# Optimization experiments

Hardware: AMD Instinct MI355X
Metric: run time of the kernel (lower is better)

The kernel has to match this reference:

```python
import jax, jax.numpy as jnp
import numpy as np

BATCH, SEQ, DIM, NH = 2, 4096, 1024, 16
HD = DIM // NH
BLOCK = 64


def setup_inputs() -> dict:
    key = jax.random.key(0)
    ks = jax.random.split(key, 8)
    x = jax.random.normal(ks[0], (BATCH, SEQ, DIM), dtype=jnp.float32)
    # standard RoPE tables: (seq, head_dim)
    inv_freq = 1.0 / (10000.0 ** (jnp.arange(0, HD, 2, dtype=jnp.float32) / HD))
    t = jnp.arange(SEQ, dtype=jnp.float32)
    freqs = jnp.outer(t, inv_freq)                      # (SEQ, HD//2)
    emb = jnp.concatenate([freqs, freqs], axis=-1)      # (SEQ, HD)
    cos, sin = jnp.cos(emb), jnp.sin(emb)
    s = 0.02
    wq = jax.random.normal(ks[1], (DIM, DIM), jnp.float32) * s
    wk = jax.random.normal(ks[2], (DIM, DIM), jnp.float32) * s
    wv = jax.random.normal(ks[3], (DIM, DIM), jnp.float32) * s
    wo = jax.random.normal(ks[4], (DIM, DIM), jnp.float32) * s
    A_log = jax.random.normal(ks[5], (NH,), jnp.float32) * 0.1
    w_dt_w = jax.random.normal(ks[6], (DIM, NH), jnp.float32) * s
    w_dt_b = jnp.zeros((NH,), jnp.float32)
    return {"x": x, "cos": cos, "sin": sin, "wq": wq, "wk": wk, "wv": wv,
            "wo": wo, "A_log": A_log, "w_dt_w": w_dt_w, "w_dt_b": w_dt_b}


def segsum(a):
    """a: (..., T) -> (..., T, T) lower-triangular segment sums, -inf above diag."""
    T = a.shape[-1]
    cs = jnp.cumsum(a, axis=-1)
    seg = cs[..., :, None] - cs[..., None, :]
    mask = jnp.tril(jnp.ones((T, T), dtype=bool))
    return jnp.where(mask, seg, -jnp.inf)


def rotate_half(t):
    t1, t2 = jnp.split(t, 2, axis=-1)
    return jnp.concatenate([-t2, t1], axis=-1)


def ssd(X, A, B, C, block_len):
    """Mamba-2 SSD chunked scan.
    X: (b,l,h,p)  A: (b,l,h)  B,C: (b,l,h,n)
    """
    b, l, h, p = X.shape
    c = l // block_len
    Xc = X.reshape(b, c, block_len, h, p)
    Bc = B.reshape(b, c, block_len, h, -1)
    Cc = C.reshape(b, c, block_len, h, -1)
    Ac = jnp.transpose(A.reshape(b, c, block_len, h), (0, 3, 1, 2))  # (b,h,c,l)
    A_cumsum = jnp.cumsum(Ac, axis=-1)
    # intra-chunk (diagonal block) output
    L = jnp.exp(segsum(Ac))                                          # (b,h,c,l,l)
    Y_diag = jnp.einsum('bclhn,bcshn,bhcls,bcshp->bclhp', Cc, Bc, L, Xc)
    # per-chunk states
    decay_states = jnp.exp(A_cumsum[:, :, :, -1:] - A_cumsum)        # (b,h,c,l)
    states = jnp.einsum('bclhn,bhcl,bclhp->bchpn', Bc, decay_states, Xc)
    init = jnp.zeros_like(states[:, :1])
    states = jnp.concatenate([init, states], axis=1)                 # (b,c+1,h,p,n)
    # inter-chunk recurrence (done as a 1-SS matmul over chunk axis)
    A_last = jnp.pad(A_cumsum[:, :, :, -1], ((0, 0), (0, 0), (1, 0)))
    decay_chunk = jnp.exp(segsum(A_last))                            # (b,h,c+1,c+1)
    new_states = jnp.einsum('bhzc,bchpn->bzhpn', decay_chunk, states)
    states, final_state = new_states[:, :-1], new_states[:, -1]
    # state -> output contribution
    state_decay_out = jnp.exp(A_cumsum)
    Y_off = jnp.einsum('bclhn,bchpn,bhcl->bclhp', Cc, states, state_decay_out)
    Y = (Y_diag + Y_off).reshape(b, l, h, p)
    return Y, final_state


def reference(x, cos, sin, wq, wk, wv, wo, A_log, w_dt_w, w_dt_b):
    b, l, dim = x.shape
    h = A_log.shape[0]
    d = dim // h
    xq = (x @ wq).reshape(b, l, h, d)
    xk = (x @ wk).reshape(b, l, h, d)
    xv = (x @ wv).reshape(b, l, h, d)
    cb = cos[None, :, None, :]
    sb = sin[None, :, None, :]
    xq = xq * cb + rotate_half(xq) * sb
    xk = xk * cb + rotate_half(xk) * sb
    dt = jax.nn.softplus(x @ w_dt_w + w_dt_b)           # (b,l,h)
    A = -jnp.exp(A_log)[None, None, :] * dt             # (b,l,h)
    X = xv * dt[..., None]                              # (b,l,h,d)
    Y, state = ssd(X, A, xk, xq, BLOCK)
    # replicate torch's transpose(1,2).view(b, l, -1) exactly:
    y = jnp.transpose(Y, (0, 2, 1, 3)).reshape(b, l, h * d)
    return y @ wo, state
```

## Files before the change

### kernel.cpp

```cpp
#include <hip/hip_runtime.h>


typedef __bf16 bf16x8 __attribute__((ext_vector_type(8)));
typedef float f32x4 __attribute__((ext_vector_type(4)));
typedef unsigned int u32x4 __attribute__((ext_vector_type(4)));
typedef unsigned short u16x8 __attribute__((ext_vector_type(8)));
typedef unsigned short u16x4 __attribute__((ext_vector_type(4)));

__device__ __forceinline__ unsigned short f2bf(float f) {
  unsigned int u = __builtin_bit_cast(unsigned int, f);
  u += 0x7fffu + ((u >> 16) & 1u);
  return (unsigned short)(u >> 16);
}
__device__ __forceinline__ float bf2f(unsigned short s) {
  unsigned int u = ((unsigned int)s) << 16;
  return __builtin_bit_cast(float, u);
}

#define GLOAD16(gp, lp)                                                \
  __builtin_amdgcn_global_load_lds(                                    \
      (const __attribute__((address_space(1))) void*)(gp),             \
      (__attribute__((address_space(3))) void*)(lp), 16, 0, 0)

__global__ __launch_bounds__(256) void prep_kernel(
    const float* __restrict__ x, unsigned short* __restrict__ x_bf,
    const float* __restrict__ wdt, unsigned short* __restrict__ wdt_bf,
    const float* __restrict__ w0, const float* __restrict__ w1,
    const float* __restrict__ w2, const float* __restrict__ w3,
    unsigned short* __restrict__ wt) {
  const int bx = blockIdx.x;
  const int tid = threadIdx.x;
  if (bx < 8192) {
    const int g = bx * 256 + tid;
    f32x4 v = *reinterpret_cast<const f32x4*>(x + (size_t)g * 4);
    u16x4 o;
    o.x = f2bf(v.x); o.y = f2bf(v.y); o.z = f2bf(v.z); o.w = f2bf(v.w);
    *reinterpret_cast<u16x4*>(x_bf + (size_t)g * 4) = o;
  } else if (bx < 8256) {
    const int g = (bx - 8192) * 256 + tid;
    const int n = g >> 10, k = g & 1023;
    wdt_bf[g] = f2bf(wdt[k * 16 + n]);
  } else {
    __shared__ float tile[32][33];
    const int t = bx - 8256;
    const int z = t >> 10, by = (t >> 5) & 31, bxx = t & 31;
    const float* w = (z == 0) ? w0 : (z == 1) ? w1 : (z == 2) ? w2 : w3;
    unsigned short* o = wt + (size_t)z * 1024 * 1024;
    const int tx = tid & 31, ty = tid >> 5;
#pragma unroll
    for (int i = 0; i < 4; ++i)
      tile[ty + i * 8][tx] = w[(size_t)(by * 32 + ty + i * 8) * 1024 + bxx * 32 + tx];
    __syncthreads();
#pragma unroll
    for (int i = 0; i < 4; ++i)
      o[(size_t)(bxx * 32 + ty + i * 8) * 1024 + by * 32 + tx] =
          f2bf(tile[tx][ty + i * 8]);
  }
}

__global__ __launch_bounds__(128) void dt_gemm_kernel(
    const unsigned short* __restrict__ A,
    const unsigned short* __restrict__ Bt,
    const float* __restrict__ bdt, float* __restrict__ dt) {
  __shared__ unsigned short As[2 * 1024];
  const int tid = threadIdx.x, lane = tid & 63, w = tid >> 6;
  const int m0 = blockIdx.x * 32;
  const unsigned short* ga =
      A + (size_t)(m0 + w * 16 + (lane >> 2)) * 1024 + (lane & 3) * 8;
  unsigned short* la = As + w * 1024;
  const int lr = lane & 15, lk = (lane >> 4) * 8;
  const unsigned short* gb = Bt + (size_t)lr * 1024 + lk;
  f32x4 acc = {};
  for (int kt = 0; kt < 1024; kt += 64) {
    GLOAD16(ga + kt, la);
    GLOAD16(ga + kt + 32, la + 512);
    bf16x8 bF0 = *reinterpret_cast<const bf16x8*>(gb + kt);
    bf16x8 bF1 = *reinterpret_cast<const bf16x8*>(gb + kt + 32);
    __syncthreads();
    bf16x8 aF0 = *reinterpret_cast<const bf16x8*>(&la[lr * 32 + lk]);
    bf16x8 aF1 = *reinterpret_cast<const bf16x8*>(&la[512 + lr * 32 + lk]);
    acc = __builtin_amdgcn_mfma_f32_16x16x32_bf16(aF0, bF0, acc, 0, 0, 0);
    acc = __builtin_amdgcn_mfma_f32_16x16x32_bf16(aF1, bF1, acc, 0, 0, 0);
    __syncthreads();
  }
  const int h = lr;
  const float bv = bdt[h];
#pragma unroll
  for (int r = 0; r < 4; ++r) {
    const int row = m0 + w * 16 + (lane >> 4) * 4 + r;
    const float a = acc[r] + bv;
    const float sp = (a > 0.f) ? (a + log1pf(expf(-a))) : log1pf(expf(a));
    dt[(size_t)row * 16 + h] = sp;
  }
}

template <int EPI>
__global__ __launch_bounds__(256) void gemm128_kernel(
    const unsigned short* __restrict__ A, const unsigned short* __restrict__ Bt,
    void* __restrict__ out0, unsigned short* __restrict__ out1,
    unsigned short* __restrict__ out2, const float* __restrict__ cosb,
    const float* __restrict__ sinb, const float* __restrict__ dtb) {
  __shared__ unsigned short As[128 * 64];
  __shared__ unsigned short Bs[128 * 64];
  const int tid = threadIdx.x, lane = tid & 63, w = tid >> 6;
  const int id = blockIdx.x + gridDim.x * blockIdx.y;
  const int cpx = (gridDim.x * gridDim.y) >> 3;
  const int swz = (id & 7) * cpx + (id >> 3);
  const int m0 = (swz / gridDim.x) * 128, n0 = (swz % gridDim.x) * 128;
  const int rw = lane >> 3;
  const int cu = ((lane & 7) ^ rw) * 8;
  const unsigned short* ga = A + (size_t)(m0 + w * 8 + rw) * 1024 + cu;
  const unsigned short* gb = Bt + (size_t)(n0 + w * 8 + rw) * 1024 + cu;
  unsigned short* la = As + (w * 8) * 64;
  unsigned short* lb = Bs + (w * 8) * 64;
  const int lr = lane & 15, lku = lane >> 4;
  const int wr = w >> 1, wc = w & 1;
  const int xr = lr & 7;
  f32x4 acc[4][4] = {};
  for (int kt = 0; kt < 1024; kt += 64) {
#pragma unroll
    for (int g = 0; g < 4; ++g) {
      GLOAD16(ga + kt + (size_t)(g * 32) * 1024, la + g * 32 * 64);
      GLOAD16(gb + kt + (size_t)(g * 32) * 1024, lb + g * 32 * 64);
    }
    __syncthreads();
#pragma unroll
    for (int kk = 0; kk < 2; ++kk) {
      const int un = (((kk * 4 + lku) ^ xr) * 8);
      bf16x8 aF[4], bF[4];
#pragma unroll
      for (int i = 0; i < 4; ++i) {
        aF[i] = *reinterpret_cast<const bf16x8*>(&As[(wr * 64 + i * 16 + lr) * 64 + un]);
        bF[i] = *reinterpret_cast<const bf16x8*>(&Bs[(wc * 64 + i * 16 + lr) * 64 + un]);
      }
#pragma unroll
      for (int i = 0; i < 4; ++i)
#pragma unroll
        for (int j = 0; j < 4; ++j)
          acc[i][j] = __builtin_amdgcn_mfma_f32_16x16x32_bf16(aF[i], bF[j], acc[i][j], 0, 0, 0);
    }
    __syncthreads();
  }
  const int r0 = m0 + wr * 64 + ((lane >> 4) << 2);
  if constexpr (EPI == 0) {
    float* O = (float*)out0;
    const int c0 = n0 + wc * 64 + lr;
#pragma unroll
    for (int i = 0; i < 4; ++i)
#pragma unroll
      for (int j = 0; j < 4; ++j)
#pragma unroll
        for (int r = 0; r < 4; ++r)
          O[(size_t)(r0 + i * 16 + r) * 1024 + c0 + j * 16] = acc[i][j][r];
  } else {
    const int col = n0 + wc * 64;
    if (col < 2048) {
      unsigned short* O = (col < 1024) ? (unsigned short*)out0 : out1;
      const int cbase = col & 1023;
#pragma unroll
      for (int i = 0; i < 4; ++i)
#pragma unroll
        for (int jj = 0; jj < 2; ++jj) {
          const int d1 = jj * 16 + lr;
#pragma unroll
          for (int r = 0; r < 4; ++r) {
            const int row = r0 + i * 16 + r;
            const int l = row & 4095;
            const float cv = cosb[(size_t)l * 64 + d1];
            const float sv = sinb[(size_t)l * 64 + d1];
            const float v1 = acc[i][jj][r], v2 = acc[i][jj + 2][r];
            O[(size_t)row * 1024 + cbase + jj * 16 + lr] = f2bf(v1 * cv - v2 * sv);
            O[(size_t)row * 1024 + cbase + jj * 16 + lr + 32] = f2bf(v2 * cv + v1 * sv);
          }
        }
    } else {
      unsigned short* O = out2;
      const int cbase = col - 2048;
      const int h = cbase >> 6;
#pragma unroll
      for (int i = 0; i < 4; ++i)
#pragma unroll
        for (int r = 0; r < 4; ++r) {
          const int row = r0 + i * 16 + r;
          const float dtv = dtb[(size_t)row * 16 + h];
#pragma unroll
          for (int j = 0; j < 4; ++j)
            O[(size_t)row * 1024 + cbase + j * 16 + lr] = f2bf(acc[i][j][r] * dtv);
        }
    }
  }
}

__global__ __launch_bounds__(256) void ssd_states_kernel(
    const unsigned short* __restrict__ Kb, const unsigned short* __restrict__ Xb,
    const float* __restrict__ dtb, const float* __restrict__ A_log,
    unsigned short* __restrict__ chunk_states, float* __restrict__ chunk_dec) {
  __shared__ unsigned short T1[64 * 72], T2[64 * 72];
  __shared__ unsigned short BtL[64 * 72], XdL[64 * 72];
  __shared__ float csL[64], decL[64];
  const int c = blockIdx.x, h = blockIdx.y, b = blockIdx.z;
  const int tid = threadIdx.x, lane = tid & 63, w = tid >> 6;
  const size_t gbase = ((size_t)(b * 4096 + c * 64)) * 1024 + h * 64;
  {
    const int s = tid >> 2, e0 = (tid & 3) * 16;
    const unsigned short* gk = Kb + gbase + (size_t)s * 1024 + e0;
    const unsigned short* gx = Xb + gbase + (size_t)s * 1024 + e0;
    *(u32x4*)&T1[s * 72 + e0] = *(const u32x4*)gk;
    *(u32x4*)&T1[s * 72 + e0 + 8] = *(const u32x4*)(gk + 8);
    *(u32x4*)&T2[s * 72 + e0] = *(const u32x4*)gx;
    *(u32x4*)&T2[s * 72 + e0 + 8] = *(const u32x4*)(gx + 8);
  }
  if (w == 0) {
    float a = -expf(A_log[h]) * dtb[((size_t)(b * 4096 + c * 64 + lane)) * 16 + h];
    float v = a;
#pragma unroll
    for (int d = 1; d < 64; d <<= 1) {
      float o = __shfl_up(v, d, 64);
      if (lane >= d) v += o;
    }
    const float tot = __shfl(v, 63, 64);
    csL[lane] = v;
    decL[lane] = expf(tot - v);
    if (lane == 0) chunk_dec[((size_t)(b * 16 + h)) * 64 + c] = expf(tot);
  }
  __syncthreads();
#pragma unroll
  for (int q = 0; q < 2; ++q) {
    const int p = lane;
    const int s0 = (q * 4 + w) * 8;
    u16x8 vb, vx;
#pragma unroll
    for (int j = 0; j < 8; ++j) {
      vb[j] = T1[(s0 + j) * 72 + p];
      vx[j] = f2bf(bf2f(T2[(s0 + j) * 72 + p]) * decL[s0 + j]);
    }
    *(u16x8*)&BtL[p * 72 + s0] = vb;
    *(u16x8*)&XdL[p * 72 + s0] = vx;
  }
  __syncthreads();
  const int lr = lane & 15, lk = (lane >> 4) * 8;
  f32x4 acc[4] = {};
#pragma unroll
  for (int kt = 0; kt < 64; kt += 32) {
    bf16x8 aF = *reinterpret_cast<const bf16x8*>(&XdL[(w * 16 + lr) * 72 + kt + lk]);
#pragma unroll
    for (int j = 0; j < 4; ++j) {
      bf16x8 bF = *reinterpret_cast<const bf16x8*>(&BtL[(j * 16 + lr) * 72 + kt + lk]);
      acc[j] = __builtin_amdgcn_mfma_f32_16x16x32_bf16(aF, bF, acc[j], 0, 0, 0);
    }
  }
  const size_t stb = ((size_t)((b * 64 + c) * 16 + h)) * 4096;
#pragma unroll
  for (int j = 0; j < 4; ++j)
#pragma unroll
    for (int r = 0; r < 4; ++r)
      chunk_states[stb + (size_t)(w * 16 + (lane >> 4) * 4 + r) * 64 + j * 16 + lr] =
          f2bf(acc[j][r]);
}

__global__ __launch_bounds__(256) void scan_kernel(
    const unsigned short* __restrict__ chunk_states, const float* __restrict__ chunk_dec,
    unsigned short* __restrict__ inc_bf, float* __restrict__ state_out) {
  __shared__ float decs[64];
  const int g = blockIdx.x * 256 + threadIdx.x;
  const int n = g & 63, p = (g >> 6) & 63, h = (g >> 12) & 15, b = g >> 16;
  if (threadIdx.x < 64)
    decs[threadIdx.x] = chunk_dec[(size_t)((blockIdx.x * 256) >> 12 & 15) * 64 +
                                  (size_t)(blockIdx.x >> 8) * 1024 + threadIdx.x];
  __syncthreads();
  const size_t pn = (size_t)p * 64 + n;
  const size_t stride = (size_t)16 * 4096;
  const size_t base0 = ((size_t)(b * 64) * 16 + h) * 4096 + pn;
  float inc = 0.f;
  float cur0 = bf2f(chunk_states[base0]);
  float cur1 = bf2f(chunk_states[base0 + stride]);
  for (int c = 0; c < 64; ++c) {
    const size_t idx = base0 + (size_t)c * stride;
    inc_bf[idx] = f2bf(inc);
    float nxt = (c < 62) ? bf2f(chunk_states[idx + 2 * stride]) : 0.f;
    inc = decs[c] * inc + cur0;
    cur0 = cur1;
    cur1 = nxt;
  }
  state_out[((size_t)(b * 16 + h) * 64 + p) * 64 + n] = inc;
}

__global__ __launch_bounds__(256) void ssd_y_kernel(
    const unsigned short* __restrict__ Qb, const unsigned short* __restrict__ Kb,
    const unsigned short* __restrict__ Xb, const unsigned short* __restrict__ Sg,
    const float* __restrict__ dtb, const float* __restrict__ A_log,
    unsigned short* __restrict__ y_bf) {
  __shared__ unsigned short Cb[64 * 72], Bb[64 * 72];
  __shared__ unsigned short Xt[64 * 72], TG[64 * 72];
  __shared__ float csL[64], sdeL[64];
  const int c = blockIdx.x, h = blockIdx.y, b = blockIdx.z;
  const int tid = threadIdx.x, lane = tid & 63, w = tid >> 6;
  const size_t gbase = ((size_t)(b * 4096 + c * 64)) * 1024 + h * 64;
  const size_t sbase = ((size_t)((b * 64 + c) * 16 + h)) * 4096;
  const unsigned short* gS = Sg + sbase;
  {
    const int s = tid >> 2, e0 = (tid & 3) * 16;
    const unsigned short* gq = Qb + gbase + (size_t)s * 1024 + e0;
    const unsigned short* gk = Kb + gbase + (size_t)s * 1024 + e0;
    const unsigned short* gx = Xb + gbase + (size_t)s * 1024 + e0;
    *(u32x4*)&Cb[s * 72 + e0] = *(const u32x4*)gq;
    *(u32x4*)&Cb[s * 72 + e0 + 8] = *(const u32x4*)(gq + 8);
    *(u32x4*)&Bb[s * 72 + e0] = *(const u32x4*)gk;
    *(u32x4*)&Bb[s * 72 + e0 + 8] = *(const u32x4*)(gk + 8);
    *(u32x4*)&TG[s * 72 + e0] = *(const u32x4*)gx;
    *(u32x4*)&TG[s * 72 + e0 + 8] = *(const u32x4*)(gx + 8);
  }
  if (w == 0) {
    float a = -expf(A_log[h]) * dtb[((size_t)(b * 4096 + c * 64 + lane)) * 16 + h];
    float v = a;
#pragma unroll
    for (int d = 1; d < 64; d <<= 1) {
      float o = __shfl_up(v, d, 64);
      if (lane >= d) v += o;
    }
    csL[lane] = v;
    sdeL[lane] = expf(v);
  }
  __syncthreads();
  const int lr = lane & 15, lk = (lane >> 4) * 8;
  f32x4 g[4] = {};
#pragma unroll
  for (int kt = 0; kt < 64; kt += 32) {
    bf16x8 aF = *reinterpret_cast<const bf16x8*>(&Cb[(w * 16 + lr) * 72 + kt + lk]);
#pragma unroll
    for (int j = 0; j < 4; ++j) {
      bf16x8 bF = *reinterpret_cast<const bf16x8*>(&Bb[(j * 16 + lr) * 72 + kt + lk]);
      g[j] = __builtin_amdgcn_mfma_f32_16x16x32_bf16(aF, bF, g[j], 0, 0, 0);
    }
  }
#pragma unroll
  for (int q = 0; q < 2; ++q) {
    const int p = lane;
    const int s0 = (q * 4 + w) * 8;
    u16x8 vx;
#pragma unroll
    for (int j = 0; j < 8; ++j) vx[j] = TG[(s0 + j) * 72 + p];
    *(u16x8*)&Xt[p * 72 + s0] = vx;
  }
  __syncthreads();
#pragma unroll
  for (int j = 0; j < 4; ++j)
#pragma unroll
    for (int r = 0; r < 4; ++r) {
      const int l = w * 16 + (lane >> 4) * 4 + r;
      const int s = j * 16 + lr;
      const float gm = (l >= s) ? g[j][r] * expf(csL[l] - csL[s]) : 0.f;
      TG[l * 72 + s] = f2bf(gm);
    }
  {
    const int rl = tid >> 2, e0 = (tid & 3) * 16;
    const float sde = sdeL[rl];
#pragma unroll
    for (int half = 0; half < 2; ++half) {
      u16x8 v = *(u16x8*)&Cb[rl * 72 + e0 + half * 8];
#pragma unroll
      for (int j = 0; j < 8; ++j) v[j] = f2bf(bf2f(v[j]) * sde);
      *(u16x8*)&Cb[rl * 72 + e0 + half * 8] = v;
    }
  }
  __syncthreads();
  f32x4 acc[4] = {};
#pragma unroll
  for (int kt = 0; kt < 64; kt += 32) {
    bf16x8 aG = *reinterpret_cast<const bf16x8*>(&TG[(w * 16 + lr) * 72 + kt + lk]);
    bf16x8 aC = *reinterpret_cast<const bf16x8*>(&Cb[(w * 16 + lr) * 72 + kt + lk]);
#pragma unroll
    for (int j = 0; j < 4; ++j) {
      bf16x8 bX = *reinterpret_cast<const bf16x8*>(&Xt[(j * 16 + lr) * 72 + kt + lk]);
      bf16x8 bS = *reinterpret_cast<const bf16x8*>(gS + (size_t)(j * 16 + lr) * 64 + kt + lk);
      acc[j] = __builtin_amdgcn_mfma_f32_16x16x32_bf16(aG, bX, acc[j], 0, 0, 0);
      acc[j] = __builtin_amdgcn_mfma_f32_16x16x32_bf16(aC, bS, acc[j], 0, 0, 0);
    }
  }
  const size_t orow = (size_t)b * 4096 + h * 256 + c * 4 + w;
#pragma unroll
  for (int j = 0; j < 4; ++j)
#pragma unroll
    for (int r = 0; r < 4; ++r) {
      const int li = (lane >> 4) * 4 + r;
      y_bf[orow * 1024 + li * 64 + j * 16 + lr] = f2bf(acc[j][r]);
    }
}

extern "C" void kernel_launch(void* const* d_in, const int* in_sizes, int n_in,
                              void* d_out, int out_size, void* d_ws, size_t ws_size,
                              hipStream_t stream) {
  (void)in_sizes; (void)n_in; (void)out_size; (void)ws_size;
  const float* x = (const float*)d_in[0];
  const float* cosb = (const float*)d_in[1];
  const float* sinb = (const float*)d_in[2];
  const float* wq = (const float*)d_in[3];
  const float* wk = (const float*)d_in[4];
  const float* wv = (const float*)d_in[5];
  const float* wo = (const float*)d_in[6];
  const float* A_log = (const float*)d_in[7];
  const float* wdt = (const float*)d_in[8];
  const float* bdt = (const float*)d_in[9];

  float* out_y = (float*)d_out;
  float* out_state = out_y + 8388608;

  const size_t MBB = 1048576;
  char* ws = (char*)d_ws;
  unsigned short* x_bf = (unsigned short*)(ws);
  unsigned short* w_t = (unsigned short*)(ws + 16 * MBB);
  unsigned short* q_bf = (unsigned short*)(ws + 24 * MBB);
  unsigned short* k_bf = (unsigned short*)(ws + 40 * MBB);
  unsigned short* xv_bf = (unsigned short*)(ws + 56 * MBB);
  float* dtb = (float*)(ws + 72 * MBB);
  unsigned short* wdt_bf = (unsigned short*)(ws + 73 * MBB);
  unsigned short* chunk_states = (unsigned short*)(ws + 74 * MBB);
  float* chunk_dec = (float*)(ws + 90 * MBB);
  unsigned short* inc_bf = (unsigned short*)(ws + 91 * MBB);

  prep_kernel<<<12352, 256, 0, stream>>>(x, x_bf, wdt, wdt_bf, wq, wk, wv, wo, w_t);
  dt_gemm_kernel<<<256, 128, 0, stream>>>(x_bf, wdt_bf, bdt, dtb);

  gemm128_kernel<3><<<dim3(24, 64), 256, 0, stream>>>(
      x_bf, w_t, q_bf, k_bf, xv_bf, cosb, sinb, dtb);

  ssd_states_kernel<<<dim3(64, 16, 2), 256, 0, stream>>>(k_bf, xv_bf, dtb, A_log,
                                                         chunk_states, chunk_dec);
  scan_kernel<<<512, 256, 0, stream>>>(chunk_states, chunk_dec, inc_bf, out_state);
  ssd_y_kernel<<<dim3(64, 16, 2), 256, 0, stream>>>(q_bf, k_bf, xv_bf, inc_bf, dtb, A_log,
                                                    x_bf );

  gemm128_kernel<0><<<dim3(8, 64), 256, 0, stream>>>(
      x_bf , w_t + 3 * MBB, out_y, nullptr, nullptr, nullptr, nullptr, nullptr);
}
```

Measured before the change: 160.0 us.

## Replace QKV GEMM with 256x256-tile, 8-wave, multi-stage async-LDS pipelined kernel

The fused QKV projection GEMM moves from 128x128 tiles with 4 waves to 256x256 tiles with 8 waves. It uses an 8-slot LDS ring filled by global_load_lds, partial vmcnt waits with barriers, and setprio around the MFMA bursts, so loads overlap compute. Larger tiles raise operand reuse per loaded byte. The wo GEMM is split into its own non-templated kernel. The risks are 128 KB of LDS and high register pressure from 128 accumulators per lane, which limit occupancy, and fewer blocks (384) on the device.

```diff
diff --git a/kernel.cpp b/kernel.cpp
--- a/kernel.cpp
+++ b/kernel.cpp
@@ -94,12 +94,118 @@
   }
 }
 
-template <int EPI>
-__global__ __launch_bounds__(256) void gemm128_kernel(
+__global__ __launch_bounds__(512, 2) void gemm256_qkv_kernel(
     const unsigned short* __restrict__ A, const unsigned short* __restrict__ Bt,
-    void* __restrict__ out0, unsigned short* __restrict__ out1,
-    unsigned short* __restrict__ out2, const float* __restrict__ cosb,
+    unsigned short* __restrict__ oq, unsigned short* __restrict__ ok,
+    unsigned short* __restrict__ ov, const float* __restrict__ cosb,
     const float* __restrict__ sinb, const float* __restrict__ dtb) {
+  __shared__ unsigned short U[8][8192];
+  const int tid = threadIdx.x, lane = tid & 63, w = tid >> 6;
+  const int wr = w >> 2, wc = w & 3;
+  const int cpx = gridDim.x >> 3;
+  const int swz = (blockIdx.x & 7) * cpx + (blockIdx.x >> 3);
+  const int m0 = (swz / 12) * 256, n0 = (swz % 12) * 256;
+  const int lr = lane & 15, l4 = lane >> 4;
+  const int sr0 = tid >> 2, su = tid & 3;
+  const int gsw = (su ^ ((sr0 >> 1) & 3)) * 8;
+  const unsigned short* gA = A + (size_t)(m0 + sr0) * 1024 + gsw;
+  const unsigned short* gB = Bt + (size_t)(n0 + sr0) * 1024 + gsw;
+  const int ko = ((l4 ^ ((lr >> 1) & 3)) * 8);
+  f32x4 acc[8][4] = {};
+
+  auto STAGE = [&](int un) {
+    const int col0 = (un >> 2) * 64 + ((un >> 1) & 1) * 32;
+    unsigned short* dst = &U[un & 7][0] + w * 512;
+    if (un & 1) {
+      GLOAD16(gB + col0, dst);
+      GLOAD16(gB + col0 + (size_t)128 * 1024, dst + 4096);
+    } else {
+      GLOAD16(gA + col0, dst);
+      GLOAD16(gA + col0 + (size_t)128 * 1024, dst + 4096);
+    }
+  };
+
+  STAGE(0); STAGE(1); STAGE(2); STAGE(3);
+
+  bf16x8 bF[4];
+#define PHASE(T, q, kk, rh, READB)                                          \
+  {                                                                         \
+    const int un = 4 * (T) + 4 + (q);                                       \
+    if (un < 64) STAGE(un);                                                 \
+    asm volatile("s_waitcnt vmcnt(6)" ::: "memory");                        \
+    __builtin_amdgcn_s_barrier();                                           \
+    asm volatile("" ::: "memory");                                          \
+    const unsigned short* sA = &U[(4 * (T) + 2 * (kk)) & 7][0];             \
+    const unsigned short* sB = &U[(4 * (T) + 2 * (kk) + 1) & 7][0];         \
+    bf16x8 aF[4];                                                           \
+    _Pragma("unroll")                                                       \
+    for (int i = 0; i < 4; ++i)                                             \
+      aF[i] = *reinterpret_cast<const bf16x8*>(                             \
+          &sA[(wr * 128 + (rh)*64 + i * 16 + lr) * 32 + ko]);               \
+    if (READB) {                                                            \
+      _Pragma("unroll")                                                     \
+      for (int j = 0; j < 4; ++j)                                           \
+        bF[j] = *reinterpret_cast<const bf16x8*>(                           \
+            &sB[(wc * 64 + j * 16 + lr) * 32 + ko]);                        \
+    }                                                                       \
+    __builtin_amdgcn_s_setprio(1);                                          \
+    _Pragma("unroll")                                                       \
+    for (int i = 0; i < 4; ++i)                                             \
+      _Pragma("unroll")                                                     \
+      for (int j = 0; j < 4; ++j)                                           \
+        acc[(rh)*4 + i][j] = __builtin_amdgcn_mfma_f32_16x16x32_bf16(       \
+            aF[i], bF[j], acc[(rh)*4 + i][j], 0, 0, 0);                     \
+    __builtin_amdgcn_s_setprio(0);                                          \
+  }
+
+  for (int T = 0; T < 16; ++T) {
+    PHASE(T, 0, 0, 0, 1);
+    PHASE(T, 1, 0, 1, 0);
+    PHASE(T, 2, 1, 0, 1);
+    PHASE(T, 3, 1, 1, 0);
+  }
+#undef PHASE
+
+  const int rbase = m0 + wr * 128 + l4 * 4;
+  const int col = n0 + wc * 64;
+  if (col < 2048) {
+    unsigned short* O = (col < 1024) ? oq : ok;
+    const int cbase = col & 1023;
+#pragma unroll
+    for (int i = 0; i < 8; ++i)
+#pragma unroll
+      for (int jj = 0; jj < 2; ++jj) {
+        const int d1 = jj * 16 + lr;
+#pragma unroll
+        for (int r = 0; r < 4; ++r) {
+          const int row = rbase + i * 16 + r;
+          const int l = row & 4095;
+          const float cv = cosb[(size_t)l * 64 + d1];
+          const float sv = sinb[(size_t)l * 64 + d1];
+          const float v1 = acc[i][jj][r], v2 = acc[i][jj + 2][r];
+          O[(size_t)row * 1024 + cbase + d1] = f2bf(v1 * cv - v2 * sv);
+          O[(size_t)row * 1024 + cbase + d1 + 32] = f2bf(v2 * cv + v1 * sv);
+        }
+      }
+  } else {
+    const int cbase = col - 2048;
+    const int h = cbase >> 6;
+#pragma unroll
+    for (int i = 0; i < 8; ++i)
+#pragma unroll
+      for (int r = 0; r < 4; ++r) {
+        const int row = rbase + i * 16 + r;
+        const float dtv = dtb[(size_t)row * 16 + h];
+#pragma unroll
+        for (int j = 0; j < 4; ++j)
+          ov[(size_t)row * 1024 + cbase + j * 16 + lr] = f2bf(acc[i][j][r] * dtv);
+      }
+  }
+}
+
+__global__ __launch_bounds__(256) void gemm128_wo_kernel(
+    const unsigned short* __restrict__ A, const unsigned short* __restrict__ Bt,
+    float* __restrict__ O) {
   __shared__ unsigned short As[128 * 64];
   __shared__ unsigned short Bs[128 * 64];
   const int tid = threadIdx.x, lane = tid & 63, w = tid >> 6;
@@ -142,53 +248,14 @@
     __syncthreads();
   }
   const int r0 = m0 + wr * 64 + ((lane >> 4) << 2);
-  if constexpr (EPI == 0) {
-    float* O = (float*)out0;
-    const int c0 = n0 + wc * 64 + lr;
-#pragma unroll
-    for (int i = 0; i < 4; ++i)
-#pragma unroll
-      for (int j = 0; j < 4; ++j)
-#pragma unroll
-        for (int r = 0; r < 4; ++r)
-          O[(size_t)(r0 + i * 16 + r) * 1024 + c0 + j * 16] = acc[i][j][r];
-  } else {
-    const int col = n0 + wc * 64;
-    if (col < 2048) {
-      unsigned short* O = (col < 1024) ? (unsigned short*)out0 : out1;
-      const int cbase = col & 1023;
-#pragma unroll
-      for (int i = 0; i < 4; ++i)
-#pragma unroll
-        for (int jj = 0; jj < 2; ++jj) {
-          const int d1 = jj * 16 + lr;
-#pragma unroll
-          for (int r = 0; r < 4; ++r) {
-            const int row = r0 + i * 16 + r;
-            const int l = row & 4095;
-            const float cv = cosb[(size_t)l * 64 + d1];
-            const float sv = sinb[(size_t)l * 64 + d1];
-            const float v1 = acc[i][jj][r], v2 = acc[i][jj + 2][r];
-            O[(size_t)row * 1024 + cbase + jj * 16 + lr] = f2bf(v1 * cv - v2 * sv);
-            O[(size_t)row * 1024 + cbase + jj * 16 + lr + 32] = f2bf(v2 * cv + v1 * sv);
-          }
-        }
-    } else {
-      unsigned short* O = out2;
-      const int cbase = col - 2048;
-      const int h = cbase >> 6;
-#pragma unroll
-      for (int i = 0; i < 4; ++i)
-#pragma unroll
-        for (int r = 0; r < 4; ++r) {
-          const int row = r0 + i * 16 + r;
-          const float dtv = dtb[(size_t)row * 16 + h];
-#pragma unroll
-          for (int j = 0; j < 4; ++j)
-            O[(size_t)row * 1024 + cbase + j * 16 + lr] = f2bf(acc[i][j][r] * dtv);
-        }
-    }
-  }
+  const int c0 = n0 + wc * 64 + lr;
+#pragma unroll
+  for (int i = 0; i < 4; ++i)
+#pragma unroll
+    for (int j = 0; j < 4; ++j)
+#pragma unroll
+      for (int r = 0; r < 4; ++r)
+        O[(size_t)(r0 + i * 16 + r) * 1024 + c0 + j * 16] = acc[i][j][r];
 }
 
 __global__ __launch_bounds__(256) void ssd_states_kernel(
@@ -421,7 +488,7 @@
   prep_kernel<<<12352, 256, 0, stream>>>(x, x_bf, wdt, wdt_bf, wq, wk, wv, wo, w_t);
   dt_gemm_kernel<<<256, 128, 0, stream>>>(x_bf, wdt_bf, bdt, dtb);
 
-  gemm128_kernel<3><<<dim3(24, 64), 256, 0, stream>>>(
+  gemm256_qkv_kernel<<<384, 512, 0, stream>>>(
       x_bf, w_t, q_bf, k_bf, xv_bf, cosb, sinb, dtb);
 
   ssd_states_kernel<<<dim3(64, 16, 2), 256, 0, stream>>>(k_bf, xv_bf, dtb, A_log,
@@ -430,6 +497,5 @@
   ssd_y_kernel<<<dim3(64, 16, 2), 256, 0, stream>>>(q_bf, k_bf, xv_bf, inc_bf, dtb, A_log,
                                                     x_bf );
 
-  gemm128_kernel<0><<<dim3(8, 64), 256, 0, stream>>>(
-      x_bf , w_t + 3 * MBB, out_y, nullptr, nullptr, nullptr, nullptr, nullptr);
-}
+  gemm128_wo_kernel<<<dim3(8, 64), 256, 0, stream>>>(x_bf , w_t + 3 * MBB, out_y);
+}
```

Result: no change. 161.5 us (+1.0%).
